# Performance work log

Hardware: AMD Instinct MI355X
Metric: run time of the kernel (lower is better)

The kernel has to match this reference:

```python
import jax, jax.numpy as jnp
import numpy as np

T, B, L, E, H = 64, 64, 2048, 128, 256  # dec steps, batch, enc len, emb, attn_size


def setup_inputs() -> dict:
    key = jax.random.key(0)
    ks = jax.random.split(key, 12)
    s = 0.1  # weight scale to keep tanh/sigmoid in a sane range
    return {
        "decoder_inputs": jax.random.normal(ks[0], (T, B, E), jnp.float32),
        "init_c": jax.random.normal(ks[1], (B, H), jnp.float32),
        "init_h": jax.random.normal(ks[2], (B, H), jnp.float32),
        "encoder_states": jax.random.normal(ks[3], (B, L, 1, H), jnp.float32),
        "enc_padding_mask": jnp.ones((B, L), jnp.float32),
        "W_x": s * jax.random.normal(ks[4], (E + H, E), jnp.float32),
        "b_x": jnp.zeros((E,), jnp.float32),
        "W_lstm": s * jax.random.normal(ks[5], (E + H, 4 * H), jnp.float32),
        "b_lstm": jnp.zeros((4 * H,), jnp.float32),
        "W_s": s * jax.random.normal(ks[6], (2 * H, H), jnp.float32),
        "b_s": jnp.zeros((H,), jnp.float32),
        "v": s * jax.random.normal(ks[7], (H,), jnp.float32),
        "w_c": s * jax.random.normal(ks[8], (H,), jnp.float32),
        "W_p": s * jax.random.normal(ks[9], (3 * H + E, 1), jnp.float32),
        "b_p": jnp.zeros((1,), jnp.float32),
        "W_o": s * jax.random.normal(ks[10], (2 * H, H), jnp.float32),
        "b_o": jnp.zeros((H,), jnp.float32),
    }


def reference(decoder_inputs, init_c, init_h, encoder_states, enc_padding_mask,
              W_x, b_x, W_lstm, b_lstm, W_s, b_s, v, w_c, W_p, b_p, W_o, b_o):
    enc = encoder_states[:, :, 0, :]            # [B, L, H]
    Hh = init_c.shape[-1]

    def step(carry, inp):
        c, h, cov, ctx = carry                  # [B,H],[B,H],[B,L],[B,H]
        # input projection: Dense(E, relu) on concat([inp, context])
        x = jax.nn.relu(jnp.concatenate([inp, ctx], -1) @ W_x + b_x)  # [B,E]
        # LSTM cell
        z = jnp.concatenate([x, h], -1) @ W_lstm + b_lstm             # [B,4H]
        i_g, f_g, g_g, o_g = jnp.split(z, 4, axis=-1)
        c = jax.nn.sigmoid(f_g) * c + jax.nn.sigmoid(i_g) * jnp.tanh(g_g)
        h = jax.nn.sigmoid(o_g) * jnp.tanh(c)
        # additive attention with coverage
        dec_feat = jnp.tanh(jnp.concatenate([c, h], -1) @ W_s + b_s)  # [B,H]
        feats = enc + dec_feat[:, None, :] + cov[:, :, None] * w_c    # [B,L,H]
        e = jnp.einsum('h,blh->bl', v, jnp.tanh(feats))               # [B,L]
        a = jax.nn.softmax(e, axis=-1) * enc_padding_mask
        a = a / jnp.sum(a, axis=1, keepdims=True)                     # renormalize
        cov = cov + a
        ctx = jnp.einsum('bl,blh->bh', a, enc)                        # [B,H]
        p_gen = jax.nn.sigmoid(
            jnp.concatenate([ctx, c, h, x], -1) @ W_p + b_p)          # [B,1]
        out = jnp.concatenate([h, ctx], -1) @ W_o + b_o               # [B,H]
        return (c, h, cov, ctx), (out, a, p_gen)

    ctx0 = jnp.zeros((init_c.shape[0], Hh), decoder_inputs.dtype)
    cov0 = jnp.zeros_like(enc_padding_mask)
    (c, h, cov, _), (outs, attns, pgens) = jax.lax.scan(
        step, (init_c, init_h, cov0, ctx0), decoder_inputs)
    return outs, c, h, attns, pgens, cov[:, :, None, None]
```

## Files before the change

### kernel.cpp

```cpp
#include <hip/hip_runtime.h>
#include <math.h>

#define T_STEPS 64
#define BB 64
#define LL 2048
#define EE 128
#define HH 256
#define NCHUNK 32
#define LCHUNK (LL / NCHUNK)

__device__ __forceinline__ float fexp(float x) {
    return __builtin_amdgcn_exp2f(x * 1.44269504088896340736f);
}
__device__ __forceinline__ float fsig(float x) {
    return __builtin_amdgcn_rcpf(1.f + __builtin_amdgcn_exp2f(-1.44269504088896340736f * x));
}
__device__ __forceinline__ float ftanh(float x) {
    float xc = fminf(fmaxf(x, -20.f), 20.f);
    float p = __builtin_amdgcn_exp2f(2.885390081777926814f * xc);
    return (p - 1.f) * __builtin_amdgcn_rcpf(p + 1.f);
}
__device__ __forceinline__ unsigned int bfr(float x) {
    unsigned int u = __float_as_uint(x);
    return (u + 0x7FFFu + ((u >> 16) & 1u)) >> 16;
}
__device__ __forceinline__ void bf8x(const uint4 q, float* f) {
    f[0] = __uint_as_float(q.x << 16); f[1] = __uint_as_float(q.x & 0xFFFF0000u);
    f[2] = __uint_as_float(q.y << 16); f[3] = __uint_as_float(q.y & 0xFFFF0000u);
    f[4] = __uint_as_float(q.z << 16); f[5] = __uint_as_float(q.z & 0xFFFF0000u);
    f[6] = __uint_as_float(q.w << 16); f[7] = __uint_as_float(q.w & 0xFFFF0000u);
}
__device__ __forceinline__ void load8(const float* p, float* d) {
    float4 a = *(const float4*)p, b = *(const float4*)(p + 4);
    d[0]=a.x; d[1]=a.y; d[2]=a.z; d[3]=a.w; d[4]=b.x; d[5]=b.y; d[6]=b.z; d[7]=b.w;
}

__global__ __launch_bounds__(256) void conv_kernel(
    const float4* __restrict__ enc, uint4* __restrict__ encb)
{
    const int n = BB * LL * HH / 8;
    for (int i = blockIdx.x * 256 + threadIdx.x; i < n; i += gridDim.x * 256) {
        const float4 a = enc[2 * i], c = enc[2 * i + 1];
        uint4 o;
        o.x = bfr(a.x) | (bfr(a.y) << 16);
        o.y = bfr(a.z) | (bfr(a.w) << 16);
        o.z = bfr(c.x) | (bfr(c.y) << 16);
        o.w = bfr(c.z) | (bfr(c.w) << 16);
        encb[i] = o;
    }
}

__global__ __launch_bounds__(512) void step_kernel(
    const float* __restrict__ dec_in,
    const float* __restrict__ init_c, const float* __restrict__ init_h,
    const float* __restrict__ sp, const float* __restrict__ ctxp,
    const float* __restrict__ Wx, const float* __restrict__ bx,
    const float* __restrict__ Wl, const float* __restrict__ bl,
    const float* __restrict__ Ws,
    float* __restrict__ ctx_hist, float* __restrict__ x_hist,
    float* __restrict__ c_hist, float* __restrict__ h_hist,
    float* __restrict__ df_part, float* __restrict__ is_ws, int t)
{
    const int b = blockIdx.x & 63;
    const int s = blockIdx.x >> 6;
    const int us = s * 64;
    const int tid = threadIdx.x;
    __shared__ float sctx[HH], siv[EE];
    __shared__ float sxh[EE + HH];
    __shared__ float red[512];
    __shared__ float scl[64], shl[64];

    const float* hsrc = (t == 0) ? init_h : h_hist + (size_t)(t - 1) * BB * HH;
    const float* csrc = (t == 0) ? init_c : c_hist + (size_t)(t - 1) * BB * HH;

    if (tid < HH) {
        if (t > 0) {
            float S = 0.f, cs = 0.f;
            #pragma unroll 8
            for (int k = 0; k < NCHUNK; ++k) {
                S += sp[k * BB + b];
                cs += ctxp[(size_t)(k * BB + b) * HH + tid];
            }
            const float invS = 1.f / S;
            const float cx = cs * invS;
            sctx[tid] = cx;
            if (s == 0) {
                ctx_hist[((size_t)(t - 1) * BB + b) * HH + tid] = cx;
                if (tid == 0) is_ws[b] = invS;
            }
        } else {
            sctx[tid] = 0.f;
        }
    } else {
        const int i = tid - HH;
        sxh[EE + i] = hsrc[(size_t)b * HH + i];
        if (i < EE && t < T_STEPS)
            siv[i] = dec_in[((size_t)t * BB + b) * EE + i];
    }
    __syncthreads();

    if (t >= T_STEPS) return;

    {
        const int j = tid & 127, q = tid >> 7;
        float a = 0.f;
        #pragma unroll 8
        for (int r = q * 96; r < q * 96 + 96; ++r) {
            const float f = (r < EE) ? siv[r] : sctx[r - EE];
            a += f * Wx[(size_t)r * EE + j];
        }
        red[tid] = a;
    }
    __syncthreads();
    if (tid < EE) {
        const float xv = fmaxf(red[tid] + red[128 + tid] + red[256 + tid]
                               + red[384 + tid] + bx[tid], 0.f);
        sxh[tid] = xv;
        if (s == 0) x_hist[((size_t)t * BB + b) * EE + tid] = xv;
    }
    __syncthreads();

    {
        const int c = tid & 255, half = tid >> 8;
        const int zcol = (c >> 6) * 256 + us + (c & 63);
        const float* w = Wl + (size_t)(half * 192) * 1024 + zcol;
        const float* f = sxh + half * 192;
        float a0 = 0.f, a1 = 0.f;
        #pragma unroll 8
        for (int r = 0; r < 96; ++r) {
            a0 += f[r] * w[(size_t)r * 1024];
            a1 += f[r + 96] * w[(size_t)(r + 96) * 1024];
        }
        red[tid] = a0 + a1;
    }
    __syncthreads();

    if (tid < 64) {
        const int u = us + tid;
        const float zi = red[tid]       + red[256 + tid] + bl[u];
        const float zf = red[64 + tid]  + red[320 + tid] + bl[256 + u];
        const float zg = red[128 + tid] + red[384 + tid] + bl[512 + u];
        const float zo = red[192 + tid] + red[448 + tid] + bl[768 + u];
        const float cp = csrc[(size_t)b * HH + u];
        const float cn = fsig(zf) * cp + fsig(zi) * ftanh(zg);
        const float hn = fsig(zo) * ftanh(cn);
        c_hist[((size_t)t * BB + b) * HH + u] = cn;
        h_hist[((size_t)t * BB + b) * HH + u] = hn;
        scl[tid] = cn;
        shl[tid] = hn;
    }
    __syncthreads();

    {
        const int j = tid & 255, half = tid >> 8;
        const float* src = half ? shl : scl;
        const int r0 = half ? (256 + us) : us;
        float a = 0.f;
        #pragma unroll 8
        for (int u = 0; u < 64; ++u)
            a += src[u] * Ws[(size_t)(r0 + u) * HH + j];
        red[tid] = a;
    }
    __syncthreads();
    if (tid < HH)
        df_part[((size_t)s * BB + b) * HH + tid] = red[tid] + red[256 + tid];
}

__global__ __launch_bounds__(256) void attn_kernel(
    const uint4* __restrict__ encb, const float* __restrict__ mask,
    float* __restrict__ cov, const float* __restrict__ df_part,
    const float* __restrict__ bs,
    const float* __restrict__ v, const float* __restrict__ wc,
    float* __restrict__ e_ws, float* __restrict__ attns,
    const float* __restrict__ is_ws,
    float* __restrict__ sp, float* __restrict__ ctxp, int t)
{
    const int prev_t = t - 1;
    const int g = blockIdx.x;
    const int b = g & (BB - 1);
    const int chunk = g >> 6;
    const int tid = threadIdx.x;
    const int wave = tid >> 6;
    const int lane = tid & 63;
    const int hc = lane & 15;
    const int lsub = lane >> 4;
    const int l0 = chunk * LCHUNK + wave * (LCHUNK / 4);

    const float* e_prev = e_ws + (size_t)(prev_t & 1) * BB * LL;
    float* e_cur = e_ws + (size_t)(t & 1) * BB * LL;
    const float iSprev = (prev_t >= 0) ? is_ws[b] : 0.f;

    float mskv[4], covv[4], epv[4];
    #pragma unroll
    for (int mi = 0; mi < 4; ++mi) {
        const int idx = b * LL + l0 + mi * 4 + lsub;
        mskv[mi] = mask[idx];
        covv[mi] = (prev_t >= 0) ? cov[idx] : 0.f;
        epv[mi]  = (prev_t >= 0) ? e_prev[idx] : 0.f;
    }

    float dfv[16], vv[16], wcv[16];
    #pragma unroll
    for (int k = 0; k < 2; ++k) {
        const int h = hc * 8 + 128 * k;
        float d0[8], d1[8], d2[8], d3[8], bsv[8];
        load8(df_part + (size_t)(0 * BB + b) * HH + h, d0);
        load8(df_part + (size_t)(1 * BB + b) * HH + h, d1);
        load8(df_part + (size_t)(2 * BB + b) * HH + h, d2);
        load8(df_part + (size_t)(3 * BB + b) * HH + h, d3);
        load8(bs + h, bsv);
        #pragma unroll
        for (int j = 0; j < 8; ++j)
            dfv[8 * k + j] = ftanh(d0[j] + d1[j] + d2[j] + d3[j] + bsv[j]);
        load8(v + h, vv + 8 * k);
        load8(wc + h, wcv + 8 * k);
    }

    float cvv[4];
    #pragma unroll
    for (int mi = 0; mi < 4; ++mi) {
        const int l = l0 + mi * 4 + lsub;
        const int idx = b * LL + l;
        if (prev_t >= 0) {
            const float a = fexp(epv[mi]) * mskv[mi] * iSprev;
            cvv[mi] = covv[mi] + a;
            if (hc == 0) {
                cov[idx] = cvv[mi];
                attns[((size_t)prev_t * BB + b) * LL + l] = a;
            }
        } else {
            cvv[mi] = 0.f;
            if (hc == 0) cov[idx] = 0.f;
        }
    }

    const uint4* ep0 = encb + (size_t)(b * LL + l0 + lsub) * 32 + hc;

    float s = 0.f;
    float cacc[16];
    #pragma unroll
    for (int j = 0; j < 16; ++j) cacc[j] = 0.f;

    uint4 eA0 = ep0[0], eA1 = ep0[16];

    #pragma unroll
    for (int mi = 0; mi < 4; ++mi) {
        uint4 eB0 = {0,0,0,0}, eB1 = {0,0,0,0};
        if (mi < 3) { eB0 = ep0[(mi + 1) * 128]; eB1 = ep0[(mi + 1) * 128 + 16]; }

        float fe[16];
        bf8x(eA0, fe); bf8x(eA1, fe + 8);
        float pp = 0.f;
        #pragma unroll
        for (int j = 0; j < 16; ++j)
            pp += vv[j] * ftanh(fe[j] + dfv[j] + cvv[mi] * wcv[j]);
        pp += __shfl_xor(pp, 1);
        pp += __shfl_xor(pp, 2);
        pp += __shfl_xor(pp, 4);
        pp += __shfl_xor(pp, 8);
        const int l = l0 + mi * 4 + lsub;
        if (hc == 0) e_cur[b * LL + l] = pp;

        const float w = fexp(pp) * mskv[mi];
        s += w;
        #pragma unroll
        for (int j = 0; j < 16; ++j) cacc[j] += w * fe[j];
        eA0 = eB0; eA1 = eB1;
    }

    #pragma unroll
    for (int off = 16; off <= 32; off <<= 1) {
        s += __shfl_xor(s, off);
        #pragma unroll
        for (int j = 0; j < 16; ++j) cacc[j] += __shfl_xor(cacc[j], off);
    }

    __shared__ float lsum[4];
    __shared__ float lctx[4][HH];
    if (lsub == 0) {
        #pragma unroll
        for (int k = 0; k < 2; ++k)
            #pragma unroll
            for (int j = 0; j < 8; ++j)
                lctx[wave][hc * 8 + 128 * k + j] = cacc[k * 8 + j];
    }
    if (lane == 0) lsum[wave] = s;
    __syncthreads();

    const int pidx = chunk * BB + b;
    ctxp[(size_t)pidx * HH + tid] =
        lctx[0][tid] + lctx[1][tid] + lctx[2][tid] + lctx[3][tid];
    if (tid == 0)
        sp[pidx] = lsum[0] + lsum[1] + lsum[2] + lsum[3];
}

__global__ __launch_bounds__(256) void epi_kernel(
    const float* __restrict__ e_ws, const float* __restrict__ mask,
    const float* __restrict__ is_ws,
    const float* __restrict__ c_hist, const float* __restrict__ h_hist,
    float* __restrict__ attns, float* __restrict__ cov,
    float* __restrict__ c_out, float* __restrict__ h_out)
{
    const int b = blockIdx.x;
    const int j = threadIdx.x;
    const float iS = is_ws[b];
    const float* e_last = e_ws + (size_t)((T_STEPS - 1) & 1) * BB * LL;
    for (int i = 0; i < LL / 256; ++i) {
        const int l = i * 256 + j;
        const int idx = b * LL + l;
        const float a = fexp(e_last[idx]) * mask[idx] * iS;
        attns[((size_t)(T_STEPS - 1) * BB + b) * LL + l] = a;
        cov[idx] += a;
    }
    c_out[b * HH + j] = c_hist[((size_t)(T_STEPS - 1) * BB + b) * HH + j];
    h_out[b * HH + j] = h_hist[((size_t)(T_STEPS - 1) * BB + b) * HH + j];
}

__global__ __launch_bounds__(512) void out_kernel(
    const float* __restrict__ h_hist, const float* __restrict__ ctx_hist,
    const float* __restrict__ c_hist, const float* __restrict__ x_hist,
    const float* __restrict__ Wo, const float* __restrict__ bo,
    const float* __restrict__ Wp, const float* __restrict__ bp,
    float* __restrict__ outs, float* __restrict__ pgens)
{
    const int t = blockIdx.x >> 3;
    const int b8 = blockIdx.x & 7;
    const int tid = threadIdx.x;
    __shared__ float hs[8 * 256], cts[8 * 256], cs2[8 * 256], xs[8 * 128];
    __shared__ float zbuf[8 * 256];

    for (int i = tid; i < 8 * 256; i += 512) {
        const int bl = i >> 8, j = i & 255;
        const size_t row = ((size_t)t * BB + b8 * 8 + bl) * HH;
        hs[i] = h_hist[row + j];
        cts[i] = ctx_hist[row + j];
        cs2[i] = c_hist[row + j];
    }
    for (int i = tid; i < 8 * 128; i += 512) {
        const int bl = i >> 7, j = i & 127;
        xs[i] = x_hist[((size_t)t * BB + b8 * 8 + bl) * EE + j];
    }
    __syncthreads();

    {
        const int j = tid & 255, rh = tid >> 8;
        float acc[8];
        #pragma unroll
        for (int bl = 0; bl < 8; ++bl) acc[bl] = 0.f;
        const int r0 = rh * 128;
        #pragma unroll 4
        for (int r = r0; r < r0 + 128; ++r) {
            const float w0 = Wo[(size_t)r * HH + j];
            const float w1 = Wo[(size_t)(256 + r) * HH + j];
            #pragma unroll
            for (int bl = 0; bl < 8; ++bl)
                acc[bl] += hs[bl * 256 + r] * w0 + cts[bl * 256 + r] * w1;
        }
        if (rh) {
            #pragma unroll
            for (int bl = 0; bl < 8; ++bl) zbuf[bl * 256 + j] = acc[bl];
        }
        __syncthreads();
        if (!rh) {
            #pragma unroll
            for (int bl = 0; bl < 8; ++bl)
                outs[((size_t)t * BB + b8 * 8 + bl) * HH + j] =
                    acc[bl] + zbuf[bl * 256 + j] + bo[j];
        }
    }

    {
        const int bl = tid >> 6, r64 = tid & 63;
        float pp = 0.f;
        for (int i = r64; i < 256; i += 64)
            pp += cts[bl * 256 + i] * Wp[i] + cs2[bl * 256 + i] * Wp[256 + i]
                + hs[bl * 256 + i] * Wp[512 + i];
        for (int i = r64; i < 128; i += 64)
            pp += xs[bl * 128 + i] * Wp[768 + i];
        #pragma unroll
        for (int off = 32; off; off >>= 1) pp += __shfl_xor(pp, off);
        if (r64 == 0)
            pgens[(size_t)t * BB + b8 * 8 + bl] = fsig(pp + bp[0]);
    }
}

extern "C" void kernel_launch(void* const* d_in, const int* in_sizes, int n_in,
                              void* d_out, int out_size, void* d_ws, size_t ws_size,
                              hipStream_t stream) {
    const float* dec_in = (const float*)d_in[0];
    const float* init_c = (const float*)d_in[1];
    const float* init_h = (const float*)d_in[2];
    const float* enc    = (const float*)d_in[3];
    const float* mask   = (const float*)d_in[4];
    const float* Wx = (const float*)d_in[5];
    const float* bx = (const float*)d_in[6];
    const float* Wl = (const float*)d_in[7];
    const float* bl = (const float*)d_in[8];
    const float* Ws = (const float*)d_in[9];
    const float* bs = (const float*)d_in[10];
    const float* v  = (const float*)d_in[11];
    const float* wc = (const float*)d_in[12];
    const float* Wp = (const float*)d_in[13];
    const float* bp = (const float*)d_in[14];
    const float* Wo = (const float*)d_in[15];
    const float* bo = (const float*)d_in[16];

    float* out   = (float*)d_out;
    float* outs  = out;
    float* c_out = outs + (size_t)T_STEPS * BB * HH;
    float* h_out = c_out + BB * HH;
    float* attns = h_out + BB * HH;
    float* pgens = attns + (size_t)T_STEPS * BB * LL;
    float* cov   = pgens + T_STEPS * BB;

    float* ws     = (float*)d_ws;
    uint4* encb   = (uint4*)ws;
    float* w      = ws + (size_t)BB * LL * HH / 2;
    float* e_ws   = w;   w += 2 * BB * LL;
    float* sp     = w;   w += NCHUNK * BB;
    float* ctxp   = w;   w += (size_t)NCHUNK * BB * HH;
    float* x_hist = w;   w += (size_t)T_STEPS * BB * EE;
    float* df_part = w;  w += 4 * BB * HH;
    float* is_ws  = w;   w += BB;
    float* ctx_hist = w; w += (size_t)T_STEPS * BB * HH;
    float* c_hist = w;   w += (size_t)T_STEPS * BB * HH;
    float* h_hist = w;   w += (size_t)T_STEPS * BB * HH;

    conv_kernel<<<4096, 256, 0, stream>>>((const float4*)enc, encb);

    for (int t = 0; t < T_STEPS; ++t) {
        step_kernel<<<256, 512, 0, stream>>>(dec_in, init_c, init_h, sp, ctxp,
            Wx, bx, Wl, bl, Ws,
            ctx_hist, x_hist, c_hist, h_hist, df_part, is_ws, t);
        attn_kernel<<<NCHUNK * BB, 256, 0, stream>>>(encb, mask, cov, df_part,
            bs, v, wc, e_ws, attns, is_ws, sp, ctxp, t);
    }
    step_kernel<<<256, 512, 0, stream>>>(dec_in, init_c, init_h, sp, ctxp,
        Wx, bx, Wl, bl, Ws,
        ctx_hist, x_hist, c_hist, h_hist, df_part, is_ws, T_STEPS);
    epi_kernel<<<BB, 256, 0, stream>>>(e_ws, mask, is_ws,
        c_hist, h_hist, attns, cov, c_out, h_out);
    out_kernel<<<512, 512, 0, stream>>>(h_hist, ctx_hist, c_hist, x_hist,
        Wo, bo, Wp, bp, outs, pgens);
}
```

Before: 2.850 ms.

## Halve attention chunk count with prefetched coverage scalars and fold epilogue into output kernel

Reduces the number of L-chunks per batch row so each attention block processes twice as many encoder rows. Per-row coverage and mask scalars are now computed inside the loop with one-step prefetch alongside the encoder loads. The separate epilogue kernel is merged into the final output kernel to save a launch. The aim is less partial-reduction traffic and launch overhead, at the cost of fewer blocks and longer per-block serial work.

```diff
diff --git a/kernel.cpp b/kernel.cpp
--- a/kernel.cpp
+++ b/kernel.cpp
@@ -6,7 +6,7 @@
 #define LL 2048
 #define EE 128
 #define HH 256
-#define NCHUNK 32
+#define NCHUNK 16
 #define LCHUNK (LL / NCHUNK)
 
 __device__ __forceinline__ float fexp(float x) {
@@ -190,15 +190,6 @@
     float* e_cur = e_ws + (size_t)(t & 1) * BB * LL;
     const float iSprev = (prev_t >= 0) ? is_ws[b] : 0.f;
 
-    float mskv[4], covv[4], epv[4];
-    #pragma unroll
-    for (int mi = 0; mi < 4; ++mi) {
-        const int idx = b * LL + l0 + mi * 4 + lsub;
-        mskv[mi] = mask[idx];
-        covv[mi] = (prev_t >= 0) ? cov[idx] : 0.f;
-        epv[mi]  = (prev_t >= 0) ? e_prev[idx] : 0.f;
-    }
-
     float dfv[16], vv[16], wcv[16];
     #pragma unroll
     for (int k = 0; k < 2; ++k) {
@@ -216,24 +207,6 @@
         load8(wc + h, wcv + 8 * k);
     }
 
-    float cvv[4];
-    #pragma unroll
-    for (int mi = 0; mi < 4; ++mi) {
-        const int l = l0 + mi * 4 + lsub;
-        const int idx = b * LL + l;
-        if (prev_t >= 0) {
-            const float a = fexp(epv[mi]) * mskv[mi] * iSprev;
-            cvv[mi] = covv[mi] + a;
-            if (hc == 0) {
-                cov[idx] = cvv[mi];
-                attns[((size_t)prev_t * BB + b) * LL + l] = a;
-            }
-        } else {
-            cvv[mi] = 0.f;
-            if (hc == 0) cov[idx] = 0.f;
-        }
-    }
-
     const uint4* ep0 = encb + (size_t)(b * LL + l0 + lsub) * 32 + hc;
 
     float s = 0.f;
@@ -241,19 +214,42 @@
     #pragma unroll
     for (int j = 0; j < 16; ++j) cacc[j] = 0.f;
 
+    auto scal = [&](int mi, float& cv, float& msk) {
+        const int l = l0 + mi * 4 + lsub;
+        const int idx = b * LL + l;
+        msk = mask[idx];
+        if (prev_t >= 0) {
+            const float a = fexp(e_prev[idx]) * msk * iSprev;
+            cv = cov[idx] + a;
+            if (hc == 0) {
+                cov[idx] = cv;
+                attns[((size_t)prev_t * BB + b) * LL + l] = a;
+            }
+        } else {
+            cv = 0.f;
+            if (hc == 0) cov[idx] = 0.f;
+        }
+    };
+
+    float cvA, mskA;
+    scal(0, cvA, mskA);
     uint4 eA0 = ep0[0], eA1 = ep0[16];
 
-    #pragma unroll
-    for (int mi = 0; mi < 4; ++mi) {
+    for (int mi = 0; mi < LCHUNK / 16; ++mi) {
+        float cvB = 0.f, mskB = 0.f;
         uint4 eB0 = {0,0,0,0}, eB1 = {0,0,0,0};
-        if (mi < 3) { eB0 = ep0[(mi + 1) * 128]; eB1 = ep0[(mi + 1) * 128 + 16]; }
+        if (mi < LCHUNK / 16 - 1) {
+            scal(mi + 1, cvB, mskB);
+            const uint4* epn = ep0 + (mi + 1) * 128;
+            eB0 = epn[0]; eB1 = epn[16];
+        }
 
         float fe[16];
         bf8x(eA0, fe); bf8x(eA1, fe + 8);
         float pp = 0.f;
         #pragma unroll
         for (int j = 0; j < 16; ++j)
-            pp += vv[j] * ftanh(fe[j] + dfv[j] + cvv[mi] * wcv[j]);
+            pp += vv[j] * ftanh(fe[j] + dfv[j] + cvA * wcv[j]);
         pp += __shfl_xor(pp, 1);
         pp += __shfl_xor(pp, 2);
         pp += __shfl_xor(pp, 4);
@@ -261,11 +257,11 @@
         const int l = l0 + mi * 4 + lsub;
         if (hc == 0) e_cur[b * LL + l] = pp;
 
-        const float w = fexp(pp) * mskv[mi];
+        const float w = fexp(pp) * mskA;
         s += w;
         #pragma unroll
         for (int j = 0; j < 16; ++j) cacc[j] += w * fe[j];
-        eA0 = eB0; eA1 = eB1;
+        cvA = cvB; mskA = mskB; eA0 = eB0; eA1 = eB1;
     }
 
     #pragma unroll
@@ -294,34 +290,16 @@
         sp[pidx] = lsum[0] + lsum[1] + lsum[2] + lsum[3];
 }
 
-__global__ __launch_bounds__(256) void epi_kernel(
-    const float* __restrict__ e_ws, const float* __restrict__ mask,
-    const float* __restrict__ is_ws,
-    const float* __restrict__ c_hist, const float* __restrict__ h_hist,
-    float* __restrict__ attns, float* __restrict__ cov,
-    float* __restrict__ c_out, float* __restrict__ h_out)
-{
-    const int b = blockIdx.x;
-    const int j = threadIdx.x;
-    const float iS = is_ws[b];
-    const float* e_last = e_ws + (size_t)((T_STEPS - 1) & 1) * BB * LL;
-    for (int i = 0; i < LL / 256; ++i) {
-        const int l = i * 256 + j;
-        const int idx = b * LL + l;
-        const float a = fexp(e_last[idx]) * mask[idx] * iS;
-        attns[((size_t)(T_STEPS - 1) * BB + b) * LL + l] = a;
-        cov[idx] += a;
-    }
-    c_out[b * HH + j] = c_hist[((size_t)(T_STEPS - 1) * BB + b) * HH + j];
-    h_out[b * HH + j] = h_hist[((size_t)(T_STEPS - 1) * BB + b) * HH + j];
-}
-
 __global__ __launch_bounds__(512) void out_kernel(
     const float* __restrict__ h_hist, const float* __restrict__ ctx_hist,
     const float* __restrict__ c_hist, const float* __restrict__ x_hist,
     const float* __restrict__ Wo, const float* __restrict__ bo,
     const float* __restrict__ Wp, const float* __restrict__ bp,
-    float* __restrict__ outs, float* __restrict__ pgens)
+    const float* __restrict__ e_ws, const float* __restrict__ mask,
+    const float* __restrict__ is_ws,
+    float* __restrict__ outs, float* __restrict__ pgens,
+    float* __restrict__ attns, float* __restrict__ cov,
+    float* __restrict__ c_out, float* __restrict__ h_out)
 {
     const int t = blockIdx.x >> 3;
     const int b8 = blockIdx.x & 7;
@@ -381,6 +359,26 @@
         for (int off = 32; off; off >>= 1) pp += __shfl_xor(pp, off);
         if (r64 == 0)
             pgens[(size_t)t * BB + b8 * 8 + bl] = fsig(pp + bp[0]);
+    }
+
+    if (t == T_STEPS - 1) {
+        const float* e_last = e_ws + (size_t)((T_STEPS - 1) & 1) * BB * LL;
+        for (int bl = 0; bl < 8; ++bl) {
+            const int b = b8 * 8 + bl;
+            const float iS = is_ws[b];
+            for (int i = tid; i < LL; i += 512) {
+                const int idx = b * LL + i;
+                const float a = fexp(e_last[idx]) * mask[idx] * iS;
+                attns[((size_t)(T_STEPS - 1) * BB + b) * LL + i] = a;
+                cov[idx] += a;
+            }
+        }
+        for (int i = tid; i < 8 * HH; i += 512) {
+            const int bl = i >> 8, j = i & 255;
+            const int b = b8 * 8 + bl;
+            c_out[(size_t)b * HH + j] = cs2[bl * 256 + j];
+            h_out[(size_t)b * HH + j] = hs[bl * 256 + j];
+        }
     }
 }
 
@@ -438,8 +436,7 @@
     step_kernel<<<256, 512, 0, stream>>>(dec_in, init_c, init_h, sp, ctxp,
         Wx, bx, Wl, bl, Ws,
         ctx_hist, x_hist, c_hist, h_hist, df_part, is_ws, T_STEPS);
-    epi_kernel<<<BB, 256, 0, stream>>>(e_ws, mask, is_ws,
-        c_hist, h_hist, attns, cov, c_out, h_out);
     out_kernel<<<512, 512, 0, stream>>>(h_hist, ctx_hist, c_hist, x_hist,
-        Wo, bo, Wp, bp, outs, pgens);
-}
+        Wo, bo, Wp, bp, e_ws, mask, is_ws,
+        outs, pgens, attns, cov, c_out, h_out);
+}
```

Result: faster. 2.711 ms (-4.9%).
